# Kernel tuning notes

Hardware: AMD Instinct MI355X
Metric: run time of the kernel (lower is better)

## Reference

```python
import jax, jax.numpy as jnp
import numpy as np

B, L, D = 4, 2048, 1024
H = 16
HD = D // H  # head_dim = 64
BASE = 10000.0


def rope_cos_sin(seq_len, head_dim, dtype=jnp.float32):
    inv_freq = 1.0 / (BASE ** (jnp.arange(0, head_dim, 2, dtype=jnp.float32) / head_dim))
    t = jnp.arange(seq_len, dtype=jnp.float32)
    freqs = jnp.outer(t, inv_freq)  # [L, HD/2]
    return jnp.cos(freqs).astype(dtype), jnp.sin(freqs).astype(dtype)


def apply_rope(x, cos, sin):
    # x: [B, H, L, HD]; cos/sin: [L, HD/2]
    x1 = x[..., ::2]
    x2 = x[..., 1::2]
    c = cos[None, None, :, :]
    s = sin[None, None, :, :]
    # NOTE: original concatenates halves (does not re-interleave)
    return jnp.concatenate([x1 * c - x2 * s, x1 * s + x2 * c], axis=-1)


def setup_inputs() -> dict:
    key = jax.random.key(0)
    k1, k2, k3 = jax.random.split(key, 3)
    x = jax.random.normal(k1, (B, L, D), dtype=jnp.float32)
    W_qkv = jax.random.normal(k2, (3 * D, D), dtype=jnp.float32) * (D ** -0.5)
    W_proj = jax.random.normal(k3, (D, D), dtype=jnp.float32) * (D ** -0.5)
    return {"x": x, "W_qkv": W_qkv, "W_proj": W_proj}


def reference(x, W_qkv, W_proj):
    b, l, d = x.shape
    scale = HD ** -0.5
    qkv = jnp.einsum('bld,ed->ble', x, W_qkv)            # [B, L, 3D]
    qkv = qkv.reshape(b, l, 3, H, HD)
    q, k, v = (jnp.transpose(qkv[:, :, i], (0, 2, 1, 3)) for i in range(3))  # [B,H,L,HD]
    cos, sin = rope_cos_sin(l, HD, x.dtype)
    q = apply_rope(q, cos, sin)
    k = apply_rope(k, cos, sin)
    attn = jnp.einsum('bhqd,bhkd->bhqk', q, k) * scale   # [B,H,L,L]
    attn = jax.nn.softmax(attn, axis=-1)
    out = jnp.einsum('bhqk,bhkd->bhqd', attn, v)         # [B,H,L,HD]
    out = jnp.transpose(out, (0, 2, 1, 3)).reshape(b, l, d)
    return jnp.einsum('bld,ed->ble', out, W_proj)
```

## Files before the change

kernel.cpp:

```cpp
#include <hip/hip_runtime.h>
#include <hip/hip_bf16.h>

typedef unsigned short u16;
typedef unsigned int u32;
typedef __attribute__((ext_vector_type(8))) short bf16x8;
typedef __attribute__((ext_vector_type(4))) float f32x4;
typedef __attribute__((ext_vector_type(2))) unsigned int u32x2;

#define NL 2048
#define NH 16

__device__ __forceinline__ u16 f2bf(float f) {
    union { __hip_bfloat16 h; u16 u; } x; x.h = __float2bfloat16(f); return x.u;
}
__device__ __forceinline__ u32 pk2(float a, float b) {
    union { float f; u32 u; } x, y; x.f = a; y.f = b;
    return ((x.u + 0x8000u) >> 16) | ((y.u + 0x8000u) & 0xffff0000u);
}
__device__ __forceinline__ u32 pkt(float lo, float hi) {
    union { float f; u32 u; } x, y; x.f = lo; y.f = hi;
    return __builtin_amdgcn_perm(y.u, x.u, 0x07060302u);
}
#if __has_builtin(__builtin_amdgcn_exp2f)
#define EXP2F(x) __builtin_amdgcn_exp2f(x)
#else
#define EXP2F(x) __expf((x) * 0.69314718056f)
#endif

__device__ __forceinline__ void quad_xchg(u32& a, u32& b) {
#if __has_builtin(__builtin_amdgcn_permlane32_swap) && __has_builtin(__builtin_amdgcn_permlane16_swap)
    u32x2 r0 = __builtin_amdgcn_permlane32_swap(a, b, false, false);
    u32x2 r1 = __builtin_amdgcn_permlane16_swap(r0.x, r0.y, false, false);
    a = r1.x; b = r1.y;
#else
    asm volatile("s_nop 1\n\t"
                 "v_permlane32_swap_b32 %0, %1\n\t"
                 "s_nop 1\n\t"
                 "v_permlane16_swap_b32 %0, %1\n\t"
                 "s_nop 1"
                 : "+v"(a), "+v"(b));
#endif
}

__device__ __forceinline__ void gload_lds16(const u16* g, u16* l) {
    __builtin_amdgcn_global_load_lds(
        (__attribute__((address_space(1))) void*)(g),
        (__attribute__((address_space(3))) void*)(l), 16, 0, 0);
}

__global__ __launch_bounds__(256) void cast_all_k(const float* __restrict__ x,
                                                  const float* __restrict__ wq,
                                                  const float* __restrict__ wp,
                                                  u16* __restrict__ xo,
                                                  u16* __restrict__ wqo,
                                                  u16* __restrict__ wpo,
                                                  float* __restrict__ cosT,
                                                  float* __restrict__ sinT) {
    if (blockIdx.x < 256) {
        int idx = blockIdx.x * 256 + threadIdx.x;
        int l = idx >> 5, i = idx & 31;
        float invf = exp2f(-(float)i * 0.41524101186092029f);
        float ang = (float)l * invf;
        cosT[idx] = cosf(ang);
        sinT[idx] = sinf(ang);
    }
    int i = blockIdx.x * 256 + threadIdx.x;
    const float* src; u16* dst; int off;
    if (i < 2097152)      { src = x;  dst = xo;  off = i; }
    else if (i < 2883584) { src = wq; dst = wqo; off = i - 2097152; }
    else                  { src = wp; dst = wpo; off = i - 2883584; }
    float4 v = *(const float4*)&src[(size_t)off * 4];
    u16 tmp[4] = {f2bf(v.x), f2bf(v.y), f2bf(v.z), f2bf(v.w)};
    *(ushort4*)&dst[(size_t)off * 4] = *(ushort4*)tmp;
}

template <typename OutT>
__global__ __launch_bounds__(256) void gemm_bt(const u16* __restrict__ A,
                                               const u16* __restrict__ Bm,
                                               OutT* __restrict__ C,
                                               int M, int N, int K) {
    __shared__ u16 As[128][64];
    __shared__ u16 Bs[128][64];
    const int t = threadIdx.x;
    const int lane = t & 63, wave = t >> 6;
    const int quad = lane >> 4, lrow = lane & 15;
    const int wr = wave >> 1, wc = wave & 1;
    const size_t m0 = (size_t)blockIdx.y * 128, n0 = (size_t)blockIdx.x * 128;

    const int srow = wave * 32 + (lane >> 3);
    const int scg  = (lane & 7) ^ (lane >> 3);

    f32x4 acc[4][4];
#pragma unroll
    for (int i = 0; i < 4; ++i)
#pragma unroll
        for (int j = 0; j < 4; ++j) acc[i][j] = (f32x4)0.0f;

    for (int k0 = 0; k0 < K; k0 += 64) {
#pragma unroll
        for (int j = 0; j < 4; ++j) {
            gload_lds16(&A[(m0 + srow + j * 8) * K + k0 + scg * 8],
                        &As[wave * 32 + j * 8][0]);
            gload_lds16(&Bm[(n0 + srow + j * 8) * K + k0 + scg * 8],
                        &Bs[wave * 32 + j * 8][0]);
        }
        __syncthreads();
#pragma unroll
        for (int ks = 0; ks < 2; ++ks) {
            bf16x8 av[4], bv[4];
#pragma unroll
            for (int i = 0; i < 4; ++i)
                av[i] = *(const bf16x8*)
                    &As[wr * 64 + i * 16 + lrow][(((ks << 2) | quad) ^ (lrow & 7)) << 3];
#pragma unroll
            for (int j = 0; j < 4; ++j)
                bv[j] = *(const bf16x8*)
                    &Bs[wc * 64 + j * 16 + lrow][(((ks << 2) | quad) ^ (lrow & 7)) << 3];
#pragma unroll
            for (int i = 0; i < 4; ++i)
#pragma unroll
                for (int j = 0; j < 4; ++j)
                    acc[i][j] = __builtin_amdgcn_mfma_f32_16x16x32_bf16(
                        av[i], bv[j], acc[i][j], 0, 0, 0);
        }
        __syncthreads();
    }
#pragma unroll
    for (int i = 0; i < 4; ++i)
#pragma unroll
        for (int r = 0; r < 4; ++r) {
            size_t row = m0 + wr * 64 + i * 16 + quad * 4 + r;
#pragma unroll
            for (int j = 0; j < 4; ++j) {
                size_t col = n0 + wc * 64 + j * 16 + lrow;
                if constexpr (sizeof(OutT) == 4)
                    C[row * N + col] = acc[i][j][r];
                else
                    C[row * N + col] = f2bf(acc[i][j][r]);
            }
        }
}

__global__ __launch_bounds__(512, 2) void gemm256_bt(const u16* __restrict__ A,
                                                     const u16* __restrict__ Bm,
                                                     u16* __restrict__ C,
                                                     int M, int N, int K) {
    __shared__ __align__(16) char smem[131072];
    const int t = threadIdx.x;
    const int lane = t & 63, w = t >> 6;
    const int quad = lane >> 4, lq = lane & 15;
    const int wm = w >> 2, wn = w & 3;
    const int rsub = lane >> 3;
    const int scg  = (lane & 7) ^ rsub;
    const size_t m0 = (size_t)blockIdx.y * 256, n0 = (size_t)blockIdx.x * 256;
    const int NT = K >> 6;

#define ASB(buf) ((u16(*)[64])(smem + (size_t)(buf) * 65536))
#define BSB(buf) ((u16(*)[64])(smem + (size_t)(buf) * 65536 + 32768))
#define STAGE_A(buf, half, kt) { \
    const size_t kro_ = (size_t)(kt) * 64 + (size_t)(scg * 8); \
    gload_lds16(&A[(m0 + (half) * 128 + w * 16 + 0 + rsub) * (size_t)K + kro_], \
                &ASB(buf)[(half) * 128 + w * 16 + 0][0]); \
    gload_lds16(&A[(m0 + (half) * 128 + w * 16 + 8 + rsub) * (size_t)K + kro_], \
                &ASB(buf)[(half) * 128 + w * 16 + 8][0]); }
#define STAGE_B(buf, half, kt) { \
    const size_t kro_ = (size_t)(kt) * 64 + (size_t)(scg * 8); \
    gload_lds16(&Bm[(n0 + (half) * 128 + w * 16 + 0 + rsub) * (size_t)K + kro_], \
                &BSB(buf)[(half) * 128 + w * 16 + 0][0]); \
    gload_lds16(&Bm[(n0 + (half) * 128 + w * 16 + 8 + rsub) * (size_t)K + kro_], \
                &BSB(buf)[(half) * 128 + w * 16 + 8][0]); }
#define RD_A(dst, rowbase) { \
    _Pragma("unroll") for (int m_ = 0; m_ < 4; ++m_) \
    _Pragma("unroll") for (int ks_ = 0; ks_ < 2; ++ks_) \
        dst[m_][ks_] = *(const bf16x8*) \
            &Ac[(rowbase) + m_ * 16 + lq][(((ks_ << 2) | quad) ^ (lq & 7)) << 3]; }
#define RD_B(dst, rowbase) { \
    _Pragma("unroll") for (int n_ = 0; n_ < 2; ++n_) \
    _Pragma("unroll") for (int ks_ = 0; ks_ < 2; ++ks_) \
        dst[n_][ks_] = *(const bf16x8*) \
            &Bc[(rowbase) + n_ * 16 + lq][(((ks_ << 2) | quad) ^ (lq & 7)) << 3]; }
#define MM(QM, QN, bvv) { \
    _Pragma("unroll") for (int m_ = 0; m_ < 4; ++m_) \
    _Pragma("unroll") for (int n_ = 0; n_ < 2; ++n_) \
    _Pragma("unroll") for (int ks_ = 0; ks_ < 2; ++ks_) \
        acc[QM][QN][m_][n_] = __builtin_amdgcn_mfma_f32_16x16x32_bf16( \
            av[m_][ks_], bvv[n_][ks_], acc[QM][QN][m_][n_], 0, 0, 0); }

    f32x4 acc[2][2][4][2];
#pragma unroll
    for (int a = 0; a < 2; ++a)
#pragma unroll
        for (int b = 0; b < 2; ++b)
#pragma unroll
            for (int m = 0; m < 4; ++m)
#pragma unroll
                for (int n = 0; n < 2; ++n) acc[a][b][m][n] = (f32x4)0.0f;
    bf16x8 av[4][2], bv0[2][2], bv1[2][2];

    STAGE_A(0, 0, 0); STAGE_B(0, 0, 0); STAGE_B(0, 1, 0); STAGE_A(0, 1, 0);
    asm volatile("s_waitcnt vmcnt(4)" ::: "memory");
    __builtin_amdgcn_s_barrier();

    for (int kt = 0; kt < NT - 1; ++kt) {
        const int cur = kt & 1, nxt = cur ^ 1;
        u16 (*Ac)[64] = ASB(cur);
        u16 (*Bc)[64] = BSB(cur);

        RD_A(av, wm * 64);
        RD_B(bv0, wn * 32);
        STAGE_A(nxt, 0, kt + 1);
        __builtin_amdgcn_s_barrier();
        __builtin_amdgcn_s_setprio(1);
        MM(0, 0, bv0);
        __builtin_amdgcn_s_setprio(0);
        asm volatile("s_waitcnt vmcnt(4)" ::: "memory");
        __builtin_amdgcn_s_barrier();

        RD_B(bv1, 128 + wn * 32);
        STAGE_B(nxt, 0, kt + 1);
        __builtin_amdgcn_s_barrier();
        __builtin_amdgcn_s_setprio(1);
        MM(0, 1, bv1);
        __builtin_amdgcn_s_setprio(0);
        asm volatile("s_waitcnt vmcnt(4)" ::: "memory");
        __builtin_amdgcn_s_barrier();

        RD_A(av, 128 + wm * 64);
        STAGE_B(nxt, 1, kt + 1);
        __builtin_amdgcn_s_barrier();
        __builtin_amdgcn_s_setprio(1);
        MM(1, 1, bv1);
        __builtin_amdgcn_s_setprio(0);
        __builtin_amdgcn_s_barrier();

        RD_B(bv0, wn * 32);
        STAGE_A(nxt, 1, kt + 1);
        __builtin_amdgcn_s_barrier();
        __builtin_amdgcn_s_setprio(1);
        MM(1, 0, bv0);
        __builtin_amdgcn_s_setprio(0);
        asm volatile("s_waitcnt vmcnt(4)" ::: "memory");
        __builtin_amdgcn_s_barrier();
    }

    {
        u16 (*Ac)[64] = ASB((NT - 1) & 1);
        u16 (*Bc)[64] = BSB((NT - 1) & 1);
        RD_A(av, wm * 64);
        RD_B(bv0, wn * 32);
        MM(0, 0, bv0);
        asm volatile("s_waitcnt vmcnt(2)" ::: "memory");
        __builtin_amdgcn_s_barrier();
        RD_B(bv1, 128 + wn * 32);
        MM(0, 1, bv1);
        asm volatile("s_waitcnt vmcnt(0)" ::: "memory");
        __builtin_amdgcn_s_barrier();
        RD_A(av, 128 + wm * 64);
        MM(1, 1, bv1);
        MM(1, 0, bv0);
    }

#pragma unroll
    for (int QM = 0; QM < 2; ++QM)
#pragma unroll
        for (int QN = 0; QN < 2; ++QN)
#pragma unroll
            for (int m = 0; m < 4; ++m)
#pragma unroll
                for (int r = 0; r < 4; ++r) {
                    size_t row = m0 + QM * 128 + wm * 64 + m * 16 + quad * 4 + r;
#pragma unroll
                    for (int n = 0; n < 2; ++n) {
                        size_t col = n0 + QN * 128 + wn * 32 + n * 16 + lq;
                        C[row * N + col] = f2bf(acc[QM][QN][m][n][r]);
                    }
                }
#undef ASB
#undef BSB
#undef STAGE_A
#undef STAGE_B
#undef RD_A
#undef RD_B
#undef MM
}

__global__ __launch_bounds__(256) void rope_vt_k(const u16* __restrict__ qkv,
                                                 const float* __restrict__ cosT,
                                                 const float* __restrict__ sinT,
                                                 u16* __restrict__ Q,
                                                 u16* __restrict__ Ko,
                                                 u16* __restrict__ VT) {
    __shared__ u16 vtile[64][72];
    const int lt = blockIdx.x, bh = blockIdx.y;
    const int b = bh >> 4, h = bh & 15;
    const int l0 = lt * 64;
    const int t = threadIdx.x;
    const float SC = 0.180336879f;
#pragma unroll
    for (int c = 0; c < 2; ++c) {
        int flat8 = c * 256 + t;
        int li = flat8 >> 3, dg = flat8 & 7;
        const u16* rowp = qkv + (size_t)(b * NL + l0 + li) * 3072 + h * 64 + dg * 8;
        uint4 qv = *(const uint4*)rowp;
        uint4 kv = *(const uint4*)(rowp + 1024);
        uint4 vv = *(const uint4*)(rowp + 2048);
        *(uint4*)&vtile[li][dg * 8] = vv;
        float4 cs = *(const float4*)&cosT[(l0 + li) * 32 + dg * 4];
        float4 sn = *(const float4*)&sinT[(l0 + li) * 32 + dg * 4];
        union { float f; u32 u; } w;
        float e0, o0, e1, o1, e2, o2, e3, o3;
        w.u = qv.x << 16; e0 = w.f; w.u = qv.x & 0xffff0000u; o0 = w.f;
        w.u = qv.y << 16; e1 = w.f; w.u = qv.y & 0xffff0000u; o1 = w.f;
        w.u = qv.z << 16; e2 = w.f; w.u = qv.z & 0xffff0000u; o2 = w.f;
        w.u = qv.w << 16; e3 = w.f; w.u = qv.w & 0xffff0000u; o3 = w.f;
        float c0 = cs.x * SC, c1 = cs.y * SC, c2 = cs.z * SC, c3 = cs.w * SC;
        float s0 = sn.x * SC, s1 = sn.y * SC, s2 = sn.z * SC, s3 = sn.w * SC;
        size_t ob = ((size_t)(b * NH + h) * NL + l0 + li) * 64;
        *(uint2*)&Q[ob + dg * 4] =
            make_uint2(pk2(e0 * c0 - o0 * s0, e1 * c1 - o1 * s1),
                       pk2(e2 * c2 - o2 * s2, e3 * c3 - o3 * s3));
        *(uint2*)&Q[ob + 32 + dg * 4] =
            make_uint2(pk2(e0 * s0 + o0 * c0, e1 * s1 + o1 * c1),
                       pk2(e2 * s2 + o2 * c2, e3 * s3 + o3 * c3));
        float f0, g0, f1, g1, f2, g2, f3, g3;
        w.u = kv.x << 16; f0 = w.f; w.u = kv.x & 0xffff0000u; g0 = w.f;
        w.u = kv.y << 16; f1 = w.f; w.u = kv.y & 0xffff0000u; g1 = w.f;
        w.u = kv.z << 16; f2 = w.f; w.u = kv.z & 0xffff0000u; g2 = w.f;
        w.u = kv.w << 16; f3 = w.f; w.u = kv.w & 0xffff0000u; g3 = w.f;
        *(uint2*)&Ko[ob + dg * 4] =
            make_uint2(pk2(f0 * cs.x - g0 * sn.x, f1 * cs.y - g1 * sn.y),
                       pk2(f2 * cs.z - g2 * sn.z, f3 * cs.w - g3 * sn.w));
        *(uint2*)&Ko[ob + 32 + dg * 4] =
            make_uint2(pk2(f0 * sn.x + g0 * cs.x, f1 * sn.y + g1 * cs.y),
                       pk2(f2 * sn.z + g2 * cs.z, f3 * sn.w + g3 * cs.w));
    }
    __syncthreads();
#pragma unroll
    for (int c = 0; c < 2; ++c) {
        int flat8 = c * 256 + t;
        int d = flat8 >> 3, lg = flat8 & 7;
        u16 tmp[8];
#pragma unroll
        for (int e = 0; e < 8; ++e) tmp[e] = vtile[lg * 8 + e][d];
        *(uint4*)&VT[((size_t)(bh * 64 + d)) * NL + l0 + lg * 8] = *(uint4*)tmp;
    }
}

__global__ __launch_bounds__(512, 4) void attn_k(const u16* __restrict__ Q,
                                                 const u16* __restrict__ Kg,
                                                 const u16* __restrict__ VT,
                                                 u16* __restrict__ Og) {
    __shared__ __align__(16) char smem[65536];
    u16 (*KsB)[64][64] = (u16(*)[64][64])(smem);
    u16 (*VsB)[64][64] = (u16(*)[64][64])(smem + 16384);
    const int t = threadIdx.x;
    const int lane = t & 63, wave = t >> 6;
    const int quad = lane >> 4, lq = lane & 15;

    const int flat = blockIdx.y * 8 + blockIdx.x;
    const int qt = (flat >> 3) & 7;
    const int bh = (flat & 7) + ((flat >> 6) << 3);
    const int q0 = qt * 256;
    const size_t qkbase = (size_t)bh * NL * 64;

    const int rsub = lane >> 3;
    const int scg  = (lane & 7) ^ rsub;

    u16 (*Qtmp)[64] = (u16(*)[64])(smem + 32768);
#pragma unroll
    for (int j = 0; j < 4; ++j)
        gload_lds16(&Q[qkbase + (size_t)(q0 + wave * 32 + j * 8 + rsub) * 64 + scg * 8],
                    &Qtmp[wave * 32 + j * 8][0]);
    const u16* kptr = Kg + qkbase + (size_t)(wave * 8 + rsub) * 64 + scg * 8;
    const u16* vptr = VT + qkbase + (size_t)(wave * 8 + rsub) * NL + scg * 8;
    gload_lds16(kptr, &KsB[0][wave * 8][0]);
    gload_lds16(vptr, &VsB[0][wave * 8][0]);
    kptr += 64 * 64;
    vptr += 64;
    __syncthreads();
    bf16x8 bq[2][2];
#pragma unroll
    for (int qh = 0; qh < 2; ++qh)
#pragma unroll
        for (int ks = 0; ks < 2; ++ks)
            bq[qh][ks] = *(const bf16x8*)
                &Qtmp[wave * 32 + qh * 16 + lq][(((ks << 2) | quad) ^ (lq & 7)) << 3];

    const bf16x8 ones = (bf16x8)(short)16256;
    f32x4 ot[2][4];
#pragma unroll
    for (int qh = 0; qh < 2; ++qh)
#pragma unroll
        for (int mt = 0; mt < 4; ++mt) ot[qh][mt] = (f32x4)0.0f;
    f32x4 lacc[2] = {(f32x4)0.0f, (f32x4)0.0f};

    for (int kc = 0; kc < NL / 64; ++kc) {
        __syncthreads();
        if (kc < NL / 64 - 1) {
            gload_lds16(kptr, &KsB[(kc + 1) & 1][wave * 8][0]);
            gload_lds16(vptr, &VsB[(kc + 1) & 1][wave * 8][0]);
            kptr += 64 * 64;
            vptr += 64;
        }
        const int cur = kc & 1;

        f32x4 st[2][4];
#pragma unroll
        for (int qh = 0; qh < 2; ++qh)
#pragma unroll
            for (int mt = 0; mt < 4; ++mt) st[qh][mt] = (f32x4)0.0f;
        __builtin_amdgcn_s_setprio(1);
#pragma unroll
        for (int half = 0; half < 2; ++half)
#pragma unroll
            for (int ks = 0; ks < 2; ++ks)
#pragma unroll
                for (int m2 = 0; m2 < 2; ++m2) {
                    const int mt = half * 2 + m2;
                    bf16x8 ak = *(const bf16x8*)
                        &KsB[cur][mt * 16 + lq][(((ks << 2) | quad) ^ (lq & 7)) << 3];
                    st[0][mt] = __builtin_amdgcn_mfma_f32_16x16x32_bf16(ak, bq[0][ks], st[0][mt], 0, 0, 0);
                    st[1][mt] = __builtin_amdgcn_mfma_f32_16x16x32_bf16(ak, bq[1][ks], st[1][mt], 0, 0, 0);
                }
        __builtin_amdgcn_s_setprio(0);

#pragma unroll
        for (int ks = 0; ks < 2; ++ks) {
            bf16x8 av[4];
#pragma unroll
            for (int mt = 0; mt < 4; ++mt)
                av[mt] = *(const bf16x8*)
                    &VsB[cur][mt * 16 + lq][(((ks << 2) | quad) ^ (lq & 7)) << 3];

            bf16x8 bp[2];
#pragma unroll
            for (int qh = 0; qh < 2; ++qh) {
                u32 a0, b0, a1, b1;
                {
                    const int mt = 2 * ks;
                    a0 = pkt(EXP2F(st[qh][mt][0]), EXP2F(st[qh][mt][1]));
                    a1 = pkt(EXP2F(st[qh][mt][2]), EXP2F(st[qh][mt][3]));
                }
                {
                    const int mt = 2 * ks + 1;
                    b0 = pkt(EXP2F(st[qh][mt][0]), EXP2F(st[qh][mt][1]));
                    b1 = pkt(EXP2F(st[qh][mt][2]), EXP2F(st[qh][mt][3]));
                }
                quad_xchg(a0, b0);
                quad_xchg(a1, b1);
                union { u32 u[4]; bf16x8 v; } bb;
                bb.u[0] = a0;
                bb.u[1] = a1;
                bb.u[2] = b0;
                bb.u[3] = b1;
                bp[qh] = bb.v;
            }

            __builtin_amdgcn_s_setprio(1);
            lacc[0] = __builtin_amdgcn_mfma_f32_16x16x32_bf16(ones, bp[0], lacc[0], 0, 0, 0);
            lacc[1] = __builtin_amdgcn_mfma_f32_16x16x32_bf16(ones, bp[1], lacc[1], 0, 0, 0);
#pragma unroll
            for (int mt = 0; mt < 4; ++mt) {
                ot[0][mt] = __builtin_amdgcn_mfma_f32_16x16x32_bf16(av[mt], bp[0], ot[0][mt], 0, 0, 0);
                ot[1][mt] = __builtin_amdgcn_mfma_f32_16x16x32_bf16(av[mt], bp[1], ot[1][mt], 0, 0, 0);
            }
            __builtin_amdgcn_s_setprio(0);
        }
    }

    __syncthreads();
    float* OT_ls = (float*)(smem + wave * 4352);
    float* Ls_ls = (float*)(smem + 34816);
    const int b = bh >> 4, h = bh & 15;
    const int qq = lane >> 2, dblk = lane & 3;
#pragma unroll
    for (int qh = 0; qh < 2; ++qh) {
#pragma unroll
        for (int mt = 0; mt < 4; ++mt)
#pragma unroll
            for (int r = 0; r < 4; ++r)
                OT_ls[(mt * 16 + quad * 4 + r) * 17 + lq] = ot[qh][mt][r];
        if (quad == 0) Ls_ls[wave * 16 + lq] = lacc[qh][0];
        __builtin_amdgcn_s_waitcnt(0xc07f);

        float rls = 1.0f / Ls_ls[wave * 16 + qq];
        u16 tmp[16];
#pragma unroll
        for (int e = 0; e < 16; ++e)
            tmp[e] = f2bf(OT_ls[(dblk * 16 + e) * 17 + qq] * rls);
        size_t orow = (size_t)b * NL + q0 + wave * 32 + qh * 16 + qq;
        size_t obase = orow * 1024 + h * 64 + dblk * 16;
        *(uint4*)&Og[obase] = *(uint4*)&tmp[0];
        *(uint4*)&Og[obase + 8] = *(uint4*)&tmp[8];
    }
}

extern "C" void kernel_launch(void* const* d_in, const int* in_sizes, int n_in,
                              void* d_out, int out_size, void* d_ws, size_t ws_size,
                              hipStream_t stream) {
    const float* x     = (const float*)d_in[0];
    const float* Wqkv  = (const float*)d_in[1];
    const float* Wproj = (const float*)d_in[2];
    float* out = (float*)d_out;

    char* ws = (char*)d_ws;
    u16* qkv     = (u16*)ws;
    u16* attnout = (u16*)ws;
    u16* Qw      = (u16*)(ws + 50331648);
    u16* Kw      = (u16*)(ws + 67108864);
    u16* VTw     = (u16*)(ws + 83886080);
    float* cosT  = (float*)(ws + 100663296);
    float* sinT  = (float*)(ws + 100925440);
    u16* x_bf    = (u16*)(ws + 101187584);
    u16* Wqkv_bf = (u16*)(ws + 117964800);
    u16* Wproj_bf= (u16*)(ws + 124256256);

    cast_all_k<<<12288, 256, 0, stream>>>(x, Wqkv, Wproj, x_bf, Wqkv_bf, Wproj_bf,
                                          cosT, sinT);
    gemm256_bt<<<dim3(12, 32), 512, 0, stream>>>(x_bf, Wqkv_bf, qkv, 8192, 3072, 1024);
    rope_vt_k<<<dim3(32, 64), 256, 0, stream>>>(qkv, cosT, sinT, Qw, Kw, VTw);
    attn_k<<<dim3(8, 64), 512, 0, stream>>>(Qw, Kw, VTw, attnout);
    gemm_bt<float><<<dim3(8, 64), 256, 0, stream>>>(attnout, Wproj_bf, out, 8192, 1024, 1024);
}
```

Before: 269.2 us.

## Shrink QKV GEMM tile to 256x128 to double block count

The QKV projection GEMM's N-tile drops from 256 to 128 columns. This doubles the grid from 384 to 768 blocks, cuts LDS use from 128KB to 96KB per block, and halves the accumulator registers. B staging now issues one load per half instead of two, and the vmcnt waits are adjusted to match. The aim is better CU occupancy and wave balance across the 256 CUs, at the cost of lower arithmetic intensity per block and more total A-matrix reloads.

```diff
diff --git a/kernel.cpp b/kernel.cpp
--- a/kernel.cpp
+++ b/kernel.cpp
@@ -9,6 +9,8 @@
 
 #define NL 2048
 #define NH 16
+
+#define BARRIER() asm volatile("s_barrier" ::: "memory")
 
 __device__ __forceinline__ u16 f2bf(float f) {
     union { __hip_bfloat16 h; u16 u; } x; x.h = __float2bfloat16(f); return x.u;
@@ -145,18 +147,18 @@
                                                      const u16* __restrict__ Bm,
                                                      u16* __restrict__ C,
                                                      int M, int N, int K) {
-    __shared__ __align__(16) char smem[131072];
+    __shared__ __align__(16) char smem[98304];
     const int t = threadIdx.x;
     const int lane = t & 63, w = t >> 6;
     const int quad = lane >> 4, lq = lane & 15;
     const int wm = w >> 2, wn = w & 3;
     const int rsub = lane >> 3;
     const int scg  = (lane & 7) ^ rsub;
-    const size_t m0 = (size_t)blockIdx.y * 256, n0 = (size_t)blockIdx.x * 256;
+    const size_t m0 = (size_t)blockIdx.y * 256, n0 = (size_t)blockIdx.x * 128;
     const int NT = K >> 6;
 
-#define ASB(buf) ((u16(*)[64])(smem + (size_t)(buf) * 65536))
-#define BSB(buf) ((u16(*)[64])(smem + (size_t)(buf) * 65536 + 32768))
+#define ASB(buf) ((u16(*)[64])(smem + (size_t)(buf) * 49152))
+#define BSB(buf) ((u16(*)[64])(smem + (size_t)(buf) * 49152 + 32768))
 #define STAGE_A(buf, half, kt) { \
     const size_t kro_ = (size_t)(kt) * 64 + (size_t)(scg * 8); \
     gload_lds16(&A[(m0 + (half) * 128 + w * 16 + 0 + rsub) * (size_t)K + kro_], \
@@ -165,41 +167,35 @@
                 &ASB(buf)[(half) * 128 + w * 16 + 8][0]); }
 #define STAGE_B(buf, half, kt) { \
     const size_t kro_ = (size_t)(kt) * 64 + (size_t)(scg * 8); \
-    gload_lds16(&Bm[(n0 + (half) * 128 + w * 16 + 0 + rsub) * (size_t)K + kro_], \
-                &BSB(buf)[(half) * 128 + w * 16 + 0][0]); \
-    gload_lds16(&Bm[(n0 + (half) * 128 + w * 16 + 8 + rsub) * (size_t)K + kro_], \
-                &BSB(buf)[(half) * 128 + w * 16 + 8][0]); }
+    gload_lds16(&Bm[(n0 + (half) * 64 + w * 8 + rsub) * (size_t)K + kro_], \
+                &BSB(buf)[(half) * 64 + w * 8][0]); }
 #define RD_A(dst, rowbase) { \
     _Pragma("unroll") for (int m_ = 0; m_ < 4; ++m_) \
     _Pragma("unroll") for (int ks_ = 0; ks_ < 2; ++ks_) \
         dst[m_][ks_] = *(const bf16x8*) \
             &Ac[(rowbase) + m_ * 16 + lq][(((ks_ << 2) | quad) ^ (lq & 7)) << 3]; }
 #define RD_B(dst, rowbase) { \
-    _Pragma("unroll") for (int n_ = 0; n_ < 2; ++n_) \
     _Pragma("unroll") for (int ks_ = 0; ks_ < 2; ++ks_) \
-        dst[n_][ks_] = *(const bf16x8*) \
-            &Bc[(rowbase) + n_ * 16 + lq][(((ks_ << 2) | quad) ^ (lq & 7)) << 3]; }
+        dst[ks_] = *(const bf16x8*) \
+            &Bc[(rowbase) + lq][(((ks_ << 2) | quad) ^ (lq & 7)) << 3]; }
 #define MM(QM, QN, bvv) { \
     _Pragma("unroll") for (int m_ = 0; m_ < 4; ++m_) \
-    _Pragma("unroll") for (int n_ = 0; n_ < 2; ++n_) \
     _Pragma("unroll") for (int ks_ = 0; ks_ < 2; ++ks_) \
-        acc[QM][QN][m_][n_] = __builtin_amdgcn_mfma_f32_16x16x32_bf16( \
-            av[m_][ks_], bvv[n_][ks_], acc[QM][QN][m_][n_], 0, 0, 0); }
-
-    f32x4 acc[2][2][4][2];
+        acc[QM][QN][m_] = __builtin_amdgcn_mfma_f32_16x16x32_bf16( \
+            av[m_][ks_], bvv[ks_], acc[QM][QN][m_], 0, 0, 0); }
+
+    f32x4 acc[2][2][4];
 #pragma unroll
     for (int a = 0; a < 2; ++a)
 #pragma unroll
         for (int b = 0; b < 2; ++b)
 #pragma unroll
-            for (int m = 0; m < 4; ++m)
-#pragma unroll
-                for (int n = 0; n < 2; ++n) acc[a][b][m][n] = (f32x4)0.0f;
-    bf16x8 av[4][2], bv0[2][2], bv1[2][2];
+            for (int m = 0; m < 4; ++m) acc[a][b][m] = (f32x4)0.0f;
+    bf16x8 av[4][2], bv0[2], bv1[2];
 
     STAGE_A(0, 0, 0); STAGE_B(0, 0, 0); STAGE_B(0, 1, 0); STAGE_A(0, 1, 0);
-    asm volatile("s_waitcnt vmcnt(4)" ::: "memory");
-    __builtin_amdgcn_s_barrier();
+    asm volatile("s_waitcnt vmcnt(3)" ::: "memory");
+    BARRIER();
 
     for (int kt = 0; kt < NT - 1; ++kt) {
         const int cur = kt & 1, nxt = cur ^ 1;
@@ -207,54 +203,54 @@
         u16 (*Bc)[64] = BSB(cur);
 
         RD_A(av, wm * 64);
-        RD_B(bv0, wn * 32);
+        RD_B(bv0, wn * 16);
         STAGE_A(nxt, 0, kt + 1);
-        __builtin_amdgcn_s_barrier();
+        BARRIER();
         __builtin_amdgcn_s_setprio(1);
         MM(0, 0, bv0);
         __builtin_amdgcn_s_setprio(0);
         asm volatile("s_waitcnt vmcnt(4)" ::: "memory");
-        __builtin_amdgcn_s_barrier();
-
-        RD_B(bv1, 128 + wn * 32);
+        BARRIER();
+
+        RD_B(bv1, 64 + wn * 16);
         STAGE_B(nxt, 0, kt + 1);
-        __builtin_amdgcn_s_barrier();
+        BARRIER();
         __builtin_amdgcn_s_setprio(1);
         MM(0, 1, bv1);
         __builtin_amdgcn_s_setprio(0);
-        asm volatile("s_waitcnt vmcnt(4)" ::: "memory");
-        __builtin_amdgcn_s_barrier();
+        asm volatile("s_waitcnt vmcnt(3)" ::: "memory");
+        BARRIER();
 
         RD_A(av, 128 + wm * 64);
         STAGE_B(nxt, 1, kt + 1);
-        __builtin_amdgcn_s_barrier();
+        BARRIER();
         __builtin_amdgcn_s_setprio(1);
         MM(1, 1, bv1);
         __builtin_amdgcn_s_setprio(0);
-        __builtin_amdgcn_s_barrier();
-
-        RD_B(bv0, wn * 32);
+        BARRIER();
+
+        RD_B(bv0, wn * 16);
         STAGE_A(nxt, 1, kt + 1);
-        __builtin_amdgcn_s_barrier();
+        BARRIER();
         __builtin_amdgcn_s_setprio(1);
         MM(1, 0, bv0);
         __builtin_amdgcn_s_setprio(0);
-        asm volatile("s_waitcnt vmcnt(4)" ::: "memory");
-        __builtin_amdgcn_s_barrier();
+        asm volatile("s_waitcnt vmcnt(3)" ::: "memory");
+        BARRIER();
     }
 
     {
         u16 (*Ac)[64] = ASB((NT - 1) & 1);
         u16 (*Bc)[64] = BSB((NT - 1) & 1);
         RD_A(av, wm * 64);
-        RD_B(bv0, wn * 32);
+        RD_B(bv0, wn * 16);
         MM(0, 0, bv0);
         asm volatile("s_waitcnt vmcnt(2)" ::: "memory");
-        __builtin_amdgcn_s_barrier();
-        RD_B(bv1, 128 + wn * 32);
+        BARRIER();
+        RD_B(bv1, 64 + wn * 16);
         MM(0, 1, bv1);
         asm volatile("s_waitcnt vmcnt(0)" ::: "memory");
-        __builtin_amdgcn_s_barrier();
+        BARRIER();
         RD_A(av, 128 + wm * 64);
         MM(1, 1, bv1);
         MM(1, 0, bv0);
@@ -269,11 +265,8 @@
 #pragma unroll
                 for (int r = 0; r < 4; ++r) {
                     size_t row = m0 + QM * 128 + wm * 64 + m * 16 + quad * 4 + r;
-#pragma unroll
-                    for (int n = 0; n < 2; ++n) {
-                        size_t col = n0 + QN * 128 + wn * 32 + n * 16 + lq;
-                        C[row * N + col] = f2bf(acc[QM][QN][m][n][r]);
-                    }
+                    size_t col = n0 + QN * 64 + wn * 16 + lq;
+                    C[row * N + col] = f2bf(acc[QM][QN][m][r]);
                 }
 #undef ASB
 #undef BSB
@@ -517,7 +510,7 @@
 
     cast_all_k<<<12288, 256, 0, stream>>>(x, Wqkv, Wproj, x_bf, Wqkv_bf, Wproj_bf,
                                           cosT, sinT);
-    gemm256_bt<<<dim3(12, 32), 512, 0, stream>>>(x_bf, Wqkv_bf, qkv, 8192, 3072, 1024);
+    gemm256_bt<<<dim3(24, 32), 512, 0, stream>>>(x_bf, Wqkv_bf, qkv, 8192, 3072, 1024);
     rope_vt_k<<<dim3(32, 64), 256, 0, stream>>>(qkv, cosT, sinT, Qw, Kw, VTw);
     attn_k<<<dim3(8, 64), 512, 0, stream>>>(Qw, Kw, VTw, attnout);
     gemm_bt<float><<<dim3(8, 64), 256, 0, stream>>>(attnout, Wproj_bf, out, 8192, 1024, 1024);
```

Measured after the change: 271.2 us. About the same (+0.7%).
